# Kernel tuning notes

Hardware: AMD Instinct MI355X
Metric: run time of the kernel (lower is better)

## Reference

```python
import jax, jax.numpy as jnp
import numpy as np

GATE_CAP = 15.0
NH = 8
DH = 128  # head_dim = embedding_dim // num_heads
EPS_BACKEND = 1e-6
EPS_NORM = 1e-6


def soft_cap(z, cap):
    return cap * jnp.tanh(z / cap)


def setup_inputs() -> dict:
    key = jax.random.key(0)
    ks = jax.random.split(key, 9)
    B, S, D = 2, 2048, 1024
    s = lambda n: (1.0 / np.sqrt(n)).astype(np.float32) if isinstance(n, np.ndarray) else np.float32(1.0 / np.sqrt(n))
    return {
        "x": jax.random.normal(ks[0], (B, S, D), jnp.float32),
        "Wq": jax.random.normal(ks[1], (D, D), jnp.float32) * s(D),
        "Wk": jax.random.normal(ks[2], (DH, D), jnp.float32) * s(D),
        "Wv": jax.random.normal(ks[3], (DH, D), jnp.float32) * s(D),
        "Wog": jax.random.normal(ks[4], (D, D), jnp.float32) * s(D),
        "Wi": jax.random.normal(ks[5], (NH, D), jnp.float32) * s(D),
        "bi": jnp.zeros((NH,), jnp.float32),
        "Wf": jax.random.normal(ks[6], (NH, D), jnp.float32) * s(D),
        "bf": jnp.ones((NH,), jnp.float32),
        "ln_w": jnp.ones((D,), jnp.float32),
        "Wout": jax.random.normal(ks[7], (D, D), jnp.float32) * s(D),
    }


def reference(x, Wq, Wk, Wv, Wog, Wi, bi, Wf, bf, ln_w, Wout):
    B, S, D = x.shape
    # projections (single weight mode, use_bias=False except gates)
    q = jnp.einsum("bsd,ed->bse", x, Wq).reshape(B, S, NH, DH).transpose(0, 2, 1, 3)  # [B,NH,S,DH]
    k = jnp.einsum("bsd,ed->bse", x, Wk)[:, None, :, :]  # [B,1,S,DH] (num_key_value_heads=1)
    v = jnp.einsum("bsd,ed->bse", x, Wv)[:, None, :, :]
    k = jnp.broadcast_to(k, (B, NH, S, DH))  # repeat_kv
    v = jnp.broadcast_to(v, (B, NH, S, DH))
    o_preact = jnp.einsum("bsd,ed->bse", x, Wog)  # [B,S,D]
    i_pre = soft_cap(jnp.einsum("bsd,hd->bhs", x, Wi) + bi[None, :, None], GATE_CAP)  # [B,NH,S]
    f_pre = soft_cap(jnp.einsum("bsd,hd->bhs", x, Wf) + bf[None, :, None], GATE_CAP)

    # native parallel mLSTM backend (stabilized), no initial state
    log_f = jax.nn.log_sigmoid(f_pre)               # [B,NH,S]
    csum = jnp.cumsum(log_f, axis=-1)
    mat_log_f = csum[:, :, :, None] - csum[:, :, None, :]  # [B,NH,S,S]
    ltr = jnp.tril(jnp.ones((S, S), dtype=bool))
    mat_log_f = jnp.where(ltr, mat_log_f, -jnp.inf)
    mat_log_d = mat_log_f + i_pre[:, :, None, :]
    vec_m = jnp.max(mat_log_d, axis=-1, keepdims=True)      # [B,NH,S,1]
    mat_d = jnp.exp(mat_log_d - vec_m)
    mat_s = jnp.einsum("bhsd,bhtd->bhst", q, k) * (DH ** -0.5)
    mat_c = mat_s * mat_d
    vec_n = jnp.maximum(jnp.abs(jnp.sum(mat_c, axis=-1, keepdims=True)), jnp.exp(-vec_m))
    C = mat_c / (vec_n + EPS_BACKEND)
    h = jnp.einsum("bhst,bhtd->bhsd", C, v)  # [B,NH,S,DH]

    # multihead layernorm (per-head, fp32 reductions, weight only)
    h = h.transpose(0, 2, 1, 3)  # [B,S,NH,DH]
    h32 = h.astype(jnp.float32)
    mu = jnp.mean(h32, axis=-1, keepdims=True)
    var = jnp.mean(jnp.square(h32 - mu), axis=-1, keepdims=True)
    h_norm = ((h32 - mu) * jax.lax.rsqrt(var + EPS_NORM)).astype(h.dtype)
    h_norm = h_norm * ln_w.reshape(NH, DH)[None, None, :, :]
    h_norm = h_norm.reshape(B, S, D)

    h_out = jax.nn.sigmoid(o_preact) * h_norm
    y = jnp.einsum("bsd,ed->bse", h_out, Wout)
    return y
```

## Files before the change

kernel.cpp:

```cpp
#include <hip/hip_runtime.h>


typedef __bf16 bf16x8 __attribute__((ext_vector_type(8)));
typedef float f32x4 __attribute__((ext_vector_type(4)));
typedef unsigned short us8 __attribute__((ext_vector_type(8)));
typedef unsigned short us4 __attribute__((ext_vector_type(4)));

__device__ __forceinline__ unsigned short f2bf(float f) {
    unsigned int u = __builtin_bit_cast(unsigned int, f);
    unsigned int r = u + 0x7fffu + ((u >> 16) & 1u);
    return (unsigned short)(r >> 16);
}
__device__ __forceinline__ float bf2f(unsigned short h) {
    unsigned int u = ((unsigned int)h) << 16;
    return __builtin_bit_cast(float, u);
}
__device__ __forceinline__ f32x4 mfma16(bf16x8 a, bf16x8 b, f32x4 c) {
    return __builtin_amdgcn_mfma_f32_16x16x32_bf16(a, b, c, 0, 0, 0);
}
__device__ __forceinline__ void gll16(const unsigned short* gsrc, unsigned short* ldst) {
    __builtin_amdgcn_global_load_lds(
        (__attribute__((address_space(1))) void*)gsrc,
        (__attribute__((address_space(3))) void*)ldst, 16, 0, 0);
}

__global__ __launch_bounds__(256) void prep(const float* __restrict__ x,
                                            const float* __restrict__ Wq,
                                            const float* __restrict__ Wk,
                                            const float* __restrict__ Wv,
                                            const float* __restrict__ Wog,
                                            const float* __restrict__ Wout,
                                            unsigned short* __restrict__ x_hi,
                                            unsigned short* __restrict__ x_lo,
                                            unsigned short* __restrict__ wc_hi,
                                            unsigned short* __restrict__ wc_lo,
                                            unsigned short* __restrict__ wo_hi,
                                            unsigned short* __restrict__ wo_lo) {
    const int id = blockIdx.x * 256 + threadIdx.x;
    f32x4 v;
    unsigned short* dh;
    unsigned short* dl;
    size_t off;
    if (id < 1048576) {
        off = (size_t)id * 4;
        v = *(const f32x4*)(x + off);
        dh = x_hi; dl = x_lo;
    } else if (id < 1048576 + 589824) {
        const int e = id - 1048576;
        const int row = e >> 8;
        const int col = (e & 255) * 4;
        off = (size_t)row * 1024 + col;
        if (row < 1024) {
            v = *(const f32x4*)(Wq + off);
#pragma unroll
            for (int t = 0; t < 4; t++) v[t] *= 0.08838834764831845f;
        } else if (row < 1152) {
            v = *(const f32x4*)(Wk + (size_t)(row - 1024) * 1024 + col);
        } else if (row < 1280) {
            v = *(const f32x4*)(Wv + (size_t)(row - 1152) * 1024 + col);
        } else {
            v = *(const f32x4*)(Wog + (size_t)(row - 1280) * 1024 + col);
        }
        dh = wc_hi; dl = wc_lo;
    } else {
        const int e = id - 1048576 - 589824;
        if (e >= 262144) return;
        off = (size_t)e * 4;
        v = *(const f32x4*)(Wout + off);
        dh = wo_hi; dl = wo_lo;
    }
    us4 h4, l4;
#pragma unroll
    for (int t = 0; t < 4; t++) {
        unsigned short hh = f2bf(v[t]);
        h4[t] = hh;
        l4[t] = f2bf(v[t] - bf2f(hh));
    }
    *(us4*)(dh + off) = h4;
    *(us4*)(dl + off) = l4;
}

__global__ __launch_bounds__(256) void gates_kernel(const float* __restrict__ x,
                                                    const float* __restrict__ Wi,
                                                    const float* __restrict__ bi,
                                                    const float* __restrict__ Wf,
                                                    const float* __restrict__ bfb,
                                                    float* __restrict__ ipre,
                                                    float* __restrict__ lgf) {
    int bs = blockIdx.x;
    int b = bs >> 11, s = bs & 2047;
    const float* xr = x + (size_t)bs * 1024;
    int lane = threadIdx.x & 63, w = threadIdx.x >> 6;
    const float* W = (w < 2) ? Wi : Wf;
    int h0 = (w & 1) * 4;
    float dot0 = 0.f, dot1 = 0.f, dot2 = 0.f, dot3 = 0.f;
    for (int i = lane; i < 1024; i += 64) {
        float xv = xr[i];
        dot0 += xv * W[(size_t)(h0 + 0) * 1024 + i];
        dot1 += xv * W[(size_t)(h0 + 1) * 1024 + i];
        dot2 += xv * W[(size_t)(h0 + 2) * 1024 + i];
        dot3 += xv * W[(size_t)(h0 + 3) * 1024 + i];
    }
#pragma unroll
    for (int o = 32; o; o >>= 1) {
        dot0 += __shfl_xor(dot0, o);
        dot1 += __shfl_xor(dot1, o);
        dot2 += __shfl_xor(dot2, o);
        dot3 += __shfl_xor(dot3, o);
    }
    if (lane == 0) {
        float d[4] = {dot0, dot1, dot2, dot3};
#pragma unroll
        for (int j = 0; j < 4; j++) {
            int hh = h0 + j;
            if (w < 2) {
                float z = d[j] + bi[hh];
                z = 15.f * tanhf(z * (1.f / 15.f));
                ipre[((size_t)b * 8 + hh) * 2048 + s] = z;
            } else {
                float z = d[j] + bfb[hh];
                z = 15.f * tanhf(z * (1.f / 15.f));
                lgf[((size_t)b * 8 + hh) * 2048 + s] = fminf(z, 0.f) - log1pf(expf(-fabsf(z)));
            }
        }
    }
}

__global__ void scan_kernel(const float* __restrict__ ipre, const float* __restrict__ lgf,
                            float* __restrict__ csum, float* __restrict__ aarr,
                            float* __restrict__ marr) {
    int bh = blockIdx.x;
    int lane = threadIdx.x;
    const float* lf = lgf + (size_t)bh * 2048;
    const float* ip = ipre + (size_t)bh * 2048;
    float* cs = csum + (size_t)bh * 2048;
    float* aa = aarr + (size_t)bh * 2048;
    float* mm = marr + (size_t)bh * 2048;
    float carry = 0.f;
    float carrym = -1e30f;
    for (int c = 0; c < 32; c++) {
        float v = lf[c * 64 + lane];
#pragma unroll
        for (int o = 1; o < 64; o <<= 1) {
            float t = __shfl_up(v, o);
            if (lane >= o) v += t;
        }
        float cval = carry + v;
        cs[c * 64 + lane] = cval;
        float a = ip[c * 64 + lane] - cval;
        aa[c * 64 + lane] = a;
        float mv = a;
#pragma unroll
        for (int o = 1; o < 64; o <<= 1) {
            float t = __shfl_up(mv, o);
            if (lane >= o) mv = fmaxf(mv, t);
        }
        float mval = fmaxf(carrym, mv);
        mm[c * 64 + lane] = mval;
        carry = __shfl(cval, 63);
        carrym = __shfl(mval, 63);
    }
}

__global__ __launch_bounds__(256) void gemm_bt3(const unsigned short* __restrict__ Ah,
                                                const unsigned short* __restrict__ Al,
                                                const unsigned short* __restrict__ Bh,
                                                const unsigned short* __restrict__ Bl,
                                                void* __restrict__ Cp,
                                                unsigned short* __restrict__ Clo,
                                                int K, int ldc, int c_bf16, int og_y0) {
    __shared__ __attribute__((aligned(16))) unsigned short Ash[128 * 32];
    __shared__ __attribute__((aligned(16))) unsigned short Asl[128 * 32];
    __shared__ __attribute__((aligned(16))) unsigned short Bsh[128 * 32];
    __shared__ __attribute__((aligned(16))) unsigned short Bsl[128 * 32];
    const int tid = threadIdx.x;
    const int lane = tid & 63, wv = tid >> 6;
    const int wr = wv >> 1, wc = wv & 1;
    const int fr = lane & 15, fg = lane >> 4;
    const bool full3 = (blockIdx.y < (unsigned)og_y0);
    const int sr = tid >> 2, sc = (tid & 3) * 8;
    const size_t abase = (size_t)(blockIdx.x * 128 + sr) * K + sc;
    const size_t bbase = (size_t)(blockIdx.y * 128 + sr) * K + sc;
    const size_t rstep = 64ull * K;
    unsigned short* a0 = &Ash[tid * 8];
    unsigned short* a1 = &Ash[2048 + tid * 8];
    unsigned short* l0 = &Asl[tid * 8];
    unsigned short* l1 = &Asl[2048 + tid * 8];
    unsigned short* b0 = &Bsh[tid * 8];
    unsigned short* b1 = &Bsh[2048 + tid * 8];
    unsigned short* m0 = &Bsl[tid * 8];
    unsigned short* m1 = &Bsl[2048 + tid * 8];
#define GLL(KT)                                                                \
    {                                                                          \
        gll16(Ah + abase + (KT), a0);                                          \
        gll16(Ah + abase + rstep + (KT), a1);                                  \
        gll16(Bh + bbase + (KT), b0);                                          \
        gll16(Bh + bbase + rstep + (KT), b1);                                  \
        if (full3) {                                                           \
            gll16(Al + abase + (KT), l0);                                      \
            gll16(Al + abase + rstep + (KT), l1);                              \
            gll16(Bl + bbase + (KT), m0);                                      \
            gll16(Bl + bbase + rstep + (KT), m1);                              \
        }                                                                      \
    }
    f32x4 acc[4][4] = {};
    GLL(0);
    for (int kt = 0; kt < K; kt += 32) {
        __syncthreads();
        bf16x8 bfh[4], bfl[4];
#pragma unroll
        for (int j = 0; j < 4; j++) {
            bfh[j] = __builtin_bit_cast(bf16x8, *(const us8*)&Bsh[(64 * wc + 16 * j + fr) * 32 + fg * 8]);
            bfl[j] = __builtin_bit_cast(bf16x8, *(const us8*)&Bsl[(64 * wc + 16 * j + fr) * 32 + fg * 8]);
        }
        __builtin_amdgcn_s_setprio(1);
        if (full3) {
#pragma unroll
            for (int i = 0; i < 4; i++) {
                bf16x8 afh = __builtin_bit_cast(bf16x8, *(const us8*)&Ash[(64 * wr + 16 * i + fr) * 32 + fg * 8]);
                bf16x8 afl = __builtin_bit_cast(bf16x8, *(const us8*)&Asl[(64 * wr + 16 * i + fr) * 32 + fg * 8]);
#pragma unroll
                for (int j = 0; j < 4; j++) {
                    acc[i][j] = mfma16(afh, bfh[j], acc[i][j]);
                    acc[i][j] = mfma16(afh, bfl[j], acc[i][j]);
                    acc[i][j] = mfma16(afl, bfh[j], acc[i][j]);
                }
            }
        } else {
#pragma unroll
            for (int i = 0; i < 4; i++) {
                bf16x8 afh = __builtin_bit_cast(bf16x8, *(const us8*)&Ash[(64 * wr + 16 * i + fr) * 32 + fg * 8]);
#pragma unroll
                for (int j = 0; j < 4; j++)
                    acc[i][j] = mfma16(afh, bfh[j], acc[i][j]);
            }
        }
        __builtin_amdgcn_s_setprio(0);
        if (kt + 32 < K) {
            __syncthreads();
            GLL(kt + 32);
        }
    }
#undef GLL
#pragma unroll
    for (int i = 0; i < 4; i++)
#pragma unroll
        for (int j = 0; j < 4; j++)
#pragma unroll
            for (int e = 0; e < 4; e++) {
                int r = blockIdx.x * 128 + 64 * wr + 16 * i + fg * 4 + e;
                int c = blockIdx.y * 128 + 64 * wc + 16 * j + fr;
                float v = acc[i][j][e];
                if (c_bf16) {
                    unsigned short h = f2bf(v);
                    ((unsigned short*)Cp)[(size_t)r * ldc + c] = h;
                    Clo[(size_t)r * ldc + c] = f2bf(v - bf2f(h));
                } else {
                    ((float*)Cp)[(size_t)r * ldc + c] = v;
                }
            }
}

__global__ __launch_bounds__(256) void make_vt(const unsigned short* __restrict__ ph,
                                               unsigned short* __restrict__ vTh) {
    __shared__ __attribute__((aligned(16))) unsigned short th[64 * 68];
    const int bid = blockIdx.x;
    const int st = bid & 31, ct = (bid >> 5) & 1, b = bid >> 6;
    const int tid = threadIdx.x;
    {
        const int sr = tid >> 2, cc = (tid & 3) * 16;
        const size_t rbase = (size_t)(b * 2048 + st * 64 + sr) * 2304 + 1152 + ct * 64 + cc;
        us8 a0 = *(const us8*)(ph + rbase);
        us8 a1 = *(const us8*)(ph + rbase + 8);
        *(us8*)&th[sr * 68 + cc] = a0;
        *(us8*)&th[sr * 68 + cc + 8] = a1;
    }
    __syncthreads();
    {
        const int cr = tid >> 2, ss = (tid & 3) * 16;
        us8 oh0, oh1;
#pragma unroll
        for (int e = 0; e < 8; e++) {
            oh0[e] = th[(ss + e) * 68 + cr];
            oh1[e] = th[(ss + 8 + e) * 68 + cr];
        }
        const size_t wbase = (size_t)b * 128 * 2048 + (size_t)(ct * 64 + cr) * 2048 + st * 64 + ss;
        *(us8*)&vTh[wbase] = oh0;
        *(us8*)&vTh[wbase + 8] = oh1;
    }
}

__global__ __launch_bounds__(256, 3) void attn_fused(const unsigned short* __restrict__ projh,
                                                     const unsigned short* __restrict__ projl,
                                                     const unsigned short* __restrict__ vTh,
                                                     const float* __restrict__ aarr,
                                                     const float* __restrict__ marr,
                                                     const float* __restrict__ csum,
                                                     const float* __restrict__ lnw,
                                                     unsigned short* __restrict__ ho_hi,
                                                     unsigned short* __restrict__ ho_lo) {
    __shared__ __attribute__((aligned(16))) unsigned short Klh[2][32 * 148];
    __shared__ __attribute__((aligned(16))) unsigned short Vlh[2][128 * 40];
    __shared__ float al[2][32];

    const int idx = blockIdx.x;
    const int half = idx >> 8;
    const int pid = idx & 255;
    const int bh = pid & 15;
    const int qt0 = pid >> 4;
    const int qt = half ? (31 - qt0) : qt0;
    const int b = bh >> 3, h = bh & 7;
    const int tid = threadIdx.x, lane = tid & 63, w = tid >> 6;
    const int fr = lane & 15, fg = lane >> 4;
    const int q0 = qt * 64;
    const int qg = q0 + 16 * w + fr;

    bf16x8 qfh[4], qfl[4];
    {
        const size_t qoff = (size_t)(b * 2048 + qg) * 2304 + h * 128;
#pragma unroll
        for (int ks = 0; ks < 4; ks++) {
            qfh[ks] = __builtin_bit_cast(bf16x8, *(const us8*)(projh + qoff + ks * 32 + fg * 8));
            qfl[ks] = __builtin_bit_cast(bf16x8, *(const us8*)(projl + qoff + ks * 32 + fg * 8));
        }
    }
    const float ma_q = marr[(size_t)bh * 2048 + qg];

    f32x4 acc[8] = {};
    float b_run = 0.f;

    const int kr = tid >> 3, kc = (tid & 7) * 16;
    const int vr = tid >> 1, vc = (tid & 1) * 16;
    const size_t kbase = (size_t)(b * 2048) * 2304 + 1024;
    const size_t vtbase = (size_t)b * 128 * 2048;

    const int nt = 2 * qt + 2;
    us8 kh0A, kh1A, vh0A, vh1A;
    us8 kh0B, kh1B, vh0B, vh1B;
    float a_stA, a_stB;
#define LOADPAIR(T0)                                                           \
    {                                                                          \
        const size_t koA = kbase + (size_t)((T0) + kr) * 2304 + kc;            \
        const size_t voA = vtbase + (size_t)vr * 2048 + (T0) + vc;             \
        kh0A = *(const us8*)(projh + koA);                                     \
        kh1A = *(const us8*)(projh + koA + 8);                                 \
        vh0A = *(const us8*)(vTh + voA);                                       \
        vh1A = *(const us8*)(vTh + voA + 8);                                   \
        a_stA = (tid < 32) ? aarr[(size_t)bh * 2048 + (T0) + tid] : 0.f;       \
        const size_t koB = koA + 32ull * 2304;                                 \
        const size_t voB = voA + 32;                                           \
        kh0B = *(const us8*)(projh + koB);                                     \
        kh1B = *(const us8*)(projh + koB + 8);                                 \
        vh0B = *(const us8*)(vTh + voB);                                       \
        vh1B = *(const us8*)(vTh + voB + 8);                                   \
        a_stB = (tid < 32) ? aarr[(size_t)bh * 2048 + (T0) + 32 + tid] : 0.f;  \
    }
#define STOREPAIR()                                                            \
    {                                                                          \
        *(us8*)&Klh[0][kr * 148 + kc] = kh0A;                                  \
        *(us8*)&Klh[0][kr * 148 + kc + 8] = kh1A;                              \
        *(us8*)&Vlh[0][vr * 40 + vc] = vh0A;                                   \
        *(us8*)&Vlh[0][vr * 40 + vc + 8] = vh1A;                               \
        *(us8*)&Klh[1][kr * 148 + kc] = kh0B;                                  \
        *(us8*)&Klh[1][kr * 148 + kc + 8] = kh1B;                              \
        *(us8*)&Vlh[1][vr * 40 + vc] = vh0B;                                   \
        *(us8*)&Vlh[1][vr * 40 + vc + 8] = vh1B;                               \
        if (tid < 32) {                                                        \
            al[0][tid] = a_stA;                                                \
            al[1][tid] = a_stB;                                                \
        }                                                                      \
    }

    LOADPAIR(0);
    STOREPAIR();
    if (nt > 2) LOADPAIR(64);
    __syncthreads();

    for (int kt = 0;;) {
        const int t0 = kt * 32;

        float djA[2][4], djB[2][4];
#pragma unroll
        for (int j = 0; j < 2; j++) {
            f32x4 sfaA = {}, sfbA = {};
            f32x4 sfaB = {}, sfbB = {};
            __builtin_amdgcn_s_setprio(1);
#pragma unroll
            for (int ks = 0; ks < 4; ks++) {
                bf16x8 kfhA = __builtin_bit_cast(bf16x8, *(const us8*)&Klh[0][(j * 16 + fr) * 148 + ks * 32 + fg * 8]);
                bf16x8 kfhB = __builtin_bit_cast(bf16x8, *(const us8*)&Klh[1][(j * 16 + fr) * 148 + ks * 32 + fg * 8]);
                sfaA = mfma16(kfhA, qfh[ks], sfaA);
                sfaB = mfma16(kfhB, qfh[ks], sfaB);
                sfbA = mfma16(kfhA, qfl[ks], sfbA);
                sfbB = mfma16(kfhB, qfl[ks], sfbB);
            }
            __builtin_amdgcn_s_setprio(0);
            f32x4 sfA = sfaA + sfbA;
            f32x4 sfB = sfaB + sfbB;
#pragma unroll
            for (int r = 0; r < 4; r++) {
                const int kloc = j * 16 + fg * 4 + r;
                const float atvA = al[0][kloc];
                const float atvB = al[1][kloc];
                djA[j][r] = ((t0 + kloc) <= qg) ? sfA[r] * __expf(atvA - ma_q) : 0.f;
                djB[j][r] = ((t0 + 32 + kloc) <= qg) ? sfB[r] * __expf(atvB - ma_q) : 0.f;
            }
        }

        {
            float tsA = djA[0][0] + djA[0][1] + djA[0][2] + djA[0][3]
                      + djA[1][0] + djA[1][1] + djA[1][2] + djA[1][3];
            tsA += __shfl_xor(tsA, 16);
            tsA += __shfl_xor(tsA, 32);
            b_run += tsA;
            float tsB = djB[0][0] + djB[0][1] + djB[0][2] + djB[0][3]
                      + djB[1][0] + djB[1][1] + djB[1][2] + djB[1][3];
            tsB += __shfl_xor(tsB, 16);
            tsB += __shfl_xor(tsB, 32);
            b_run += tsB;
        }

        const int srlo = 32 * ((lane >> 4) & 1) + fr;
        {
            float p8[8];
#pragma unroll
            for (int e = 0; e < 8; e++) {
                const int sl = srlo + ((e >= 4) ? 16 : 0);
                const float v0 = __shfl(djA[0][e & 3], sl);
                const float v1 = __shfl(djA[1][e & 3], sl);
                p8[e] = (lane & 32) ? v1 : v0;
            }
            us8 phu, plu;
#pragma unroll
            for (int e = 0; e < 8; e++) {
                unsigned short hh = f2bf(p8[e]);
                phu[e] = hh;
                plu[e] = f2bf(p8[e] - bf2f(hh));
            }
            const bf16x8 pfh = __builtin_bit_cast(bf16x8, phu);
            const bf16x8 pfl = __builtin_bit_cast(bf16x8, plu);
            __builtin_amdgcn_s_setprio(1);
#pragma unroll
            for (int jb = 0; jb < 8; jb++) {
                bf16x8 vfh = __builtin_bit_cast(bf16x8, *(const us8*)&Vlh[0][(jb * 16 + fr) * 40 + fg * 8]);
                acc[jb] = mfma16(vfh, pfh, acc[jb]);
                acc[jb] = mfma16(vfh, pfl, acc[jb]);
            }
            __builtin_amdgcn_s_setprio(0);
        }
        {
            float p8[8];
#pragma unroll
            for (int e = 0; e < 8; e++) {
                const int sl = srlo + ((e >= 4) ? 16 : 0);
                const float v0 = __shfl(djB[0][e & 3], sl);
                const float v1 = __shfl(djB[1][e & 3], sl);
                p8[e] = (lane & 32) ? v1 : v0;
            }
            us8 phu, plu;
#pragma unroll
            for (int e = 0; e < 8; e++) {
                unsigned short hh = f2bf(p8[e]);
                phu[e] = hh;
                plu[e] = f2bf(p8[e] - bf2f(hh));
            }
            const bf16x8 pfh = __builtin_bit_cast(bf16x8, phu);
            const bf16x8 pfl = __builtin_bit_cast(bf16x8, plu);
            __builtin_amdgcn_s_setprio(1);
#pragma unroll
            for (int jb = 0; jb < 8; jb++) {
                bf16x8 vfh = __builtin_bit_cast(bf16x8, *(const us8*)&Vlh[1][(jb * 16 + fr) * 40 + fg * 8]);
                acc[jb] = mfma16(vfh, pfh, acc[jb]);
                acc[jb] = mfma16(vfh, pfl, acc[jb]);
            }
            __builtin_amdgcn_s_setprio(0);
        }

        kt += 2;
        if (kt >= nt) break;
        __syncthreads();
        STOREPAIR();
        if (kt + 2 < nt) LOADPAIR((kt + 2) * 32);
        __syncthreads();
    }
#undef LOADPAIR
#undef STOREPAIR

    const float cs_q = csum[(size_t)bh * 2048 + qg];
    const float nf = __expf(-(cs_q + ma_q));
    const float n = fmaxf(fabsf(b_run), nf);
    const float inv = 1.f / (n + 1e-6f);
#pragma unroll
    for (int jb = 0; jb < 8; jb++) acc[jb] *= inv;

    float s1 = 0.f;
#pragma unroll
    for (int jb = 0; jb < 8; jb++) s1 += acc[jb][0] + acc[jb][1] + acc[jb][2] + acc[jb][3];
    s1 += __shfl_xor(s1, 16);
    s1 += __shfl_xor(s1, 32);
    const float mu = s1 * (1.f / 128.f);
    float vv = 0.f;
#pragma unroll
    for (int jb = 0; jb < 8; jb++)
#pragma unroll
        for (int e = 0; e < 4; e++) {
            float d = acc[jb][e] - mu;
            vv += d * d;
        }
    vv += __shfl_xor(vv, 16);
    vv += __shfl_xor(vv, 32);
    const float rstd = rsqrtf(vv * (1.f / 128.f) + 1e-6f);

    const size_t obase = (size_t)(b * 2048 + qg) * 2304 + 1280 + h * 128 + fg * 4;
    const size_t hbase = (size_t)(b * 2048 + qg) * 1024 + h * 128 + fg * 4;
#pragma unroll
    for (int jb = 0; jb < 8; jb++) {
        us4 ogh = *(const us4*)(projh + obase + jb * 16);
        us4 ogl = *(const us4*)(projl + obase + jb * 16);
        f32x4 lw = *(const f32x4*)&lnw[h * 128 + jb * 16 + fg * 4];
        us4 hi4, lo4;
#pragma unroll
        for (int e = 0; e < 4; e++) {
            const float og = bf2f(ogh[e]) + bf2f(ogl[e]);
            const float sig = 1.f / (1.f + __expf(-og));
            const float ho = (acc[jb][e] - mu) * rstd * lw[e] * sig;
            unsigned short h1 = f2bf(ho);
            hi4[e] = h1;
            lo4[e] = f2bf(ho - bf2f(h1));
        }
        *(us4*)&ho_hi[hbase + jb * 16] = hi4;
        *(us4*)&ho_lo[hbase + jb * 16] = lo4;
    }
}

extern "C" void kernel_launch(void* const* d_in, const int* in_sizes, int n_in,
                              void* d_out, int out_size, void* d_ws, size_t ws_size,
                              hipStream_t stream) {
    (void)in_sizes; (void)n_in; (void)out_size; (void)ws_size;
    const float* x    = (const float*)d_in[0];
    const float* Wq   = (const float*)d_in[1];
    const float* Wk   = (const float*)d_in[2];
    const float* Wv   = (const float*)d_in[3];
    const float* Wog  = (const float*)d_in[4];
    const float* Wi   = (const float*)d_in[5];
    const float* bi   = (const float*)d_in[6];
    const float* Wf   = (const float*)d_in[7];
    const float* bfb  = (const float*)d_in[8];
    const float* lnw  = (const float*)d_in[9];
    const float* Wout = (const float*)d_in[10];

    char* p = (char*)d_ws;
    auto carve = [&](size_t bytes) -> char* {
        char* r = p;
        p += (bytes + 255) & ~(size_t)255;
        return r;
    };
    unsigned short* x_hi   = (unsigned short*)carve(4194304ull * 2);
    unsigned short* x_lo   = (unsigned short*)carve(4194304ull * 2);
    unsigned short* wc_hi  = (unsigned short*)carve(2359296ull * 2);
    unsigned short* wc_lo  = (unsigned short*)carve(2359296ull * 2);
    unsigned short* wo_hi  = (unsigned short*)carve(1048576ull * 2);
    unsigned short* wo_lo  = (unsigned short*)carve(1048576ull * 2);
    unsigned short* pr_hi  = (unsigned short*)carve(4096ull * 2304 * 2);
    unsigned short* pr_lo  = (unsigned short*)carve(4096ull * 2304 * 2);
    unsigned short* vT_hi  = (unsigned short*)carve(524288ull * 2);
    float* ipre    = (float*)carve(32768ull * 4);
    float* lgf_buf = (float*)carve(32768ull * 4);
    float* csum    = (float*)carve(32768ull * 4);
    float* aarr    = (float*)carve(32768ull * 4);
    float* marr    = (float*)carve(32768ull * 4);
    unsigned short* ho_hi = x_hi;
    unsigned short* ho_lo = x_lo;

    prep<<<7424, 256, 0, stream>>>(x, Wq, Wk, Wv, Wog, Wout,
                                   x_hi, x_lo, wc_hi, wc_lo, wo_hi, wo_lo);
    gates_kernel<<<4096, 256, 0, stream>>>(x, Wi, bi, Wf, bfb, ipre, lgf_buf);
    scan_kernel<<<16, 64, 0, stream>>>(ipre, lgf_buf, csum, aarr, marr);
    gemm_bt3<<<dim3(32, 18), 256, 0, stream>>>(x_hi, x_lo, wc_hi, wc_lo, pr_hi, pr_lo, 1024, 2304, 1, 10);
    make_vt<<<128, 256, 0, stream>>>(pr_hi, vT_hi);
    attn_fused<<<512, 256, 0, stream>>>(pr_hi, pr_lo, vT_hi, aarr, marr, csum, lnw, ho_hi, ho_lo);
    gemm_bt3<<<dim3(32, 8), 256, 0, stream>>>(ho_hi, ho_lo, wo_hi, wo_lo, d_out, nullptr, 1024, 1024, 0, 1000);
}
```

Baseline: 305.9 us.

## Double-buffer K/V LDS tiles in attention loop to drop one barrier

```diff
diff --git a/kernel.cpp b/kernel.cpp
--- a/kernel.cpp
+++ b/kernel.cpp
@@ -290,7 +290,7 @@
     }
 }
 
-__global__ __launch_bounds__(256, 3) void attn_fused(const unsigned short* __restrict__ projh,
+__global__ __launch_bounds__(256, 2) void attn_fused(const unsigned short* __restrict__ projh,
                                                      const unsigned short* __restrict__ projl,
                                                      const unsigned short* __restrict__ vTh,
                                                      const float* __restrict__ aarr,
@@ -299,9 +299,9 @@
                                                      const float* __restrict__ lnw,
                                                      unsigned short* __restrict__ ho_hi,
                                                      unsigned short* __restrict__ ho_lo) {
-    __shared__ __attribute__((aligned(16))) unsigned short Klh[2][32 * 148];
-    __shared__ __attribute__((aligned(16))) unsigned short Vlh[2][128 * 40];
-    __shared__ float al[2][32];
+    __shared__ __attribute__((aligned(16))) unsigned short Klh[4][32 * 148];
+    __shared__ __attribute__((aligned(16))) unsigned short Vlh[4][128 * 40];
+    __shared__ float al[4][32];
 
     const int idx = blockIdx.x;
     const int half = idx >> 8;
@@ -334,50 +334,58 @@
     const size_t kbase = (size_t)(b * 2048) * 2304 + 1024;
     const size_t vtbase = (size_t)b * 128 * 2048;
 
-    const int nt = 2 * qt + 2;
+    const int npairs = qt + 1;
     us8 kh0A, kh1A, vh0A, vh1A;
     us8 kh0B, kh1B, vh0B, vh1B;
     float a_stA, a_stB;
-#define LOADPAIR(T0)                                                           \
+#define LOADPAIR(P)                                                            \
     {                                                                          \
-        const size_t koA = kbase + (size_t)((T0) + kr) * 2304 + kc;            \
-        const size_t voA = vtbase + (size_t)vr * 2048 + (T0) + vc;             \
+        const int T0 = (P) * 64;                                               \
+        const size_t koA = kbase + (size_t)(T0 + kr) * 2304 + kc;              \
+        const size_t voA = vtbase + (size_t)vr * 2048 + T0 + vc;               \
         kh0A = *(const us8*)(projh + koA);                                     \
         kh1A = *(const us8*)(projh + koA + 8);                                 \
         vh0A = *(const us8*)(vTh + voA);                                       \
         vh1A = *(const us8*)(vTh + voA + 8);                                   \
-        a_stA = (tid < 32) ? aarr[(size_t)bh * 2048 + (T0) + tid] : 0.f;       \
+        a_stA = (tid < 32) ? aarr[(size_t)bh * 2048 + T0 + tid] : 0.f;         \
         const size_t koB = koA + 32ull * 2304;                                 \
         const size_t voB = voA + 32;                                           \
         kh0B = *(const us8*)(projh + koB);                                     \
         kh1B = *(const us8*)(projh + koB + 8);                                 \
         vh0B = *(const us8*)(vTh + voB);                                       \
         vh1B = *(const us8*)(vTh + voB + 8);                                   \
-        a_stB = (tid < 32) ? aarr[(size_t)bh * 2048 + (T0) + 32 + tid] : 0.f;  \
-    }
-#define STOREPAIR()                                                            \
+        a_stB = (tid < 32) ? aarr[(size_t)bh * 2048 + T0 + 32 + tid] : 0.f;    \
+    }
+#define STOREPAIR(S)                                                           \
     {                                                                          \
-        *(us8*)&Klh[0][kr * 148 + kc] = kh0A;                                  \
-        *(us8*)&Klh[0][kr * 148 + kc + 8] = kh1A;                              \
-        *(us8*)&Vlh[0][vr * 40 + vc] = vh0A;                                   \
-        *(us8*)&Vlh[0][vr * 40 + vc + 8] = vh1A;                               \
-        *(us8*)&Klh[1][kr * 148 + kc] = kh0B;                                  \
-        *(us8*)&Klh[1][kr * 148 + kc + 8] = kh1B;                              \
-        *(us8*)&Vlh[1][vr * 40 + vc] = vh0B;                                   \
-        *(us8*)&Vlh[1][vr * 40 + vc + 8] = vh1B;                               \
+        const int bA = 2 * (S), bB = 2 * (S) + 1;                              \
+        *(us8*)&Klh[bA][kr * 148 + kc] = kh0A;                                 \
+        *(us8*)&Klh[bA][kr * 148 + kc + 8] = kh1A;                             \
+        *(us8*)&Vlh[bA][vr * 40 + vc] = vh0A;                                  \
+        *(us8*)&Vlh[bA][vr * 40 + vc + 8] = vh1A;                              \
+        *(us8*)&Klh[bB][kr * 148 + kc] = kh0B;                                 \
+        *(us8*)&Klh[bB][kr * 148 + kc + 8] = kh1B;                             \
+        *(us8*)&Vlh[bB][vr * 40 + vc] = vh0B;                                  \
+        *(us8*)&Vlh[bB][vr * 40 + vc + 8] = vh1B;                              \
         if (tid < 32) {                                                        \
-            al[0][tid] = a_stA;                                                \
-            al[1][tid] = a_stB;                                                \
+            al[bA][tid] = a_stA;                                               \
+            al[bB][tid] = a_stB;                                               \
         }                                                                      \
     }
 
     LOADPAIR(0);
-    STOREPAIR();
-    if (nt > 2) LOADPAIR(64);
+    STOREPAIR(0);
+    if (npairs > 1) LOADPAIR(1);
     __syncthreads();
 
-    for (int kt = 0;;) {
-        const int t0 = kt * 32;
+    for (int p = 0;;) {
+        const int cur = p & 1;
+        const int bA = 2 * cur, bB = 2 * cur + 1;
+        const int t0 = p * 64;
+        if (p + 1 < npairs) {
+            STOREPAIR((p + 1) & 1);
+            if (p + 2 < npairs) LOADPAIR(p + 2);
+        }
 
         float djA[2][4], djB[2][4];
 #pragma unroll
@@ -387,8 +395,8 @@
             __builtin_amdgcn_s_setprio(1);
 #pragma unroll
             for (int ks = 0; ks < 4; ks++) {
-                bf16x8 kfhA = __builtin_bit_cast(bf16x8, *(const us8*)&Klh[0][(j * 16 + fr) * 148 + ks * 32 + fg * 8]);
-                bf16x8 kfhB = __builtin_bit_cast(bf16x8, *(const us8*)&Klh[1][(j * 16 + fr) * 148 + ks * 32 + fg * 8]);
+                bf16x8 kfhA = __builtin_bit_cast(bf16x8, *(const us8*)&Klh[bA][(j * 16 + fr) * 148 + ks * 32 + fg * 8]);
+                bf16x8 kfhB = __builtin_bit_cast(bf16x8, *(const us8*)&Klh[bB][(j * 16 + fr) * 148 + ks * 32 + fg * 8]);
                 sfaA = mfma16(kfhA, qfh[ks], sfaA);
                 sfaB = mfma16(kfhB, qfh[ks], sfaB);
                 sfbA = mfma16(kfhA, qfl[ks], sfbA);
@@ -400,8 +408,8 @@
 #pragma unroll
             for (int r = 0; r < 4; r++) {
                 const int kloc = j * 16 + fg * 4 + r;
-                const float atvA = al[0][kloc];
-                const float atvB = al[1][kloc];
+                const float atvA = al[bA][kloc];
+                const float atvB = al[bB][kloc];
                 djA[j][r] = ((t0 + kloc) <= qg) ? sfA[r] * __expf(atvA - ma_q) : 0.f;
                 djB[j][r] = ((t0 + 32 + kloc) <= qg) ? sfB[r] * __expf(atvB - ma_q) : 0.f;
             }
@@ -442,7 +450,7 @@
             __builtin_amdgcn_s_setprio(1);
 #pragma unroll
             for (int jb = 0; jb < 8; jb++) {
-                bf16x8 vfh = __builtin_bit_cast(bf16x8, *(const us8*)&Vlh[0][(jb * 16 + fr) * 40 + fg * 8]);
+                bf16x8 vfh = __builtin_bit_cast(bf16x8, *(const us8*)&Vlh[bA][(jb * 16 + fr) * 40 + fg * 8]);
                 acc[jb] = mfma16(vfh, pfh, acc[jb]);
                 acc[jb] = mfma16(vfh, pfl, acc[jb]);
             }
@@ -469,18 +477,15 @@
             __builtin_amdgcn_s_setprio(1);
 #pragma unroll
             for (int jb = 0; jb < 8; jb++) {
-                bf16x8 vfh = __builtin_bit_cast(bf16x8, *(const us8*)&Vlh[1][(jb * 16 + fr) * 40 + fg * 8]);
+                bf16x8 vfh = __builtin_bit_cast(bf16x8, *(const us8*)&Vlh[bB][(jb * 16 + fr) * 40 + fg * 8]);
                 acc[jb] = mfma16(vfh, pfh, acc[jb]);
                 acc[jb] = mfma16(vfh, pfl, acc[jb]);
             }
             __builtin_amdgcn_s_setprio(0);
         }
 
-        kt += 2;
-        if (kt >= nt) break;
-        __syncthreads();
-        STOREPAIR();
-        if (kt + 2 < nt) LOADPAIR((kt + 2) * 32);
+        p++;
+        if (p >= npairs) break;
         __syncthreads();
     }
 #undef LOADPAIR
```

Result: faster. 284.7 us, median of 2 (-6.9%).
